# Kernel optimization log

Hardware: AMD Instinct MI355X
Metric: run time of the kernel (lower is better)

## Reference

```python
import jax, jax.numpy as jnp
import numpy as np

NQ = 200000; K = 4; M = 64; KEY = 64; V = 128; E = 64; B = 512; S = 200

def setup_inputs() -> dict:
    key = jax.random.key(0)
    ks = jax.random.split(key, 16)
    return {
        'q_embed_table': jax.random.normal(ks[0], (NQ + 1, E), jnp.float32) * 0.1,
        'alpha_mean': jax.random.normal(ks[1], (NQ,), jnp.float32) * 0.2,
        'beta_base': jax.random.normal(ks[2], (NQ,), jnp.float32) * 0.5,
        'beta_gaps': jax.random.uniform(ks[3], (NQ, K - 2), jnp.float32) * 0.5 + 0.25,
        'ability_means': jax.random.normal(ks[4], (M, V), jnp.float32) * 0.1,
        'ability_log_vars': jnp.zeros((M, V), jnp.float32),
        'memory_keys': jax.random.normal(ks[5], (M, KEY), jnp.float32),
        'q_to_key_w': jax.random.normal(ks[6], (E, KEY), jnp.float32) / np.sqrt(E),
        'q_to_key_b': jnp.zeros((KEY,), jnp.float32),
        'qa_embed_w': jax.random.normal(ks[7], (2, E), jnp.float32),
        'qa_embed_b': jnp.zeros((E,), jnp.float32),
        'qa_to_ev_w': jax.random.normal(ks[8], (E, V), jnp.float32) / np.sqrt(E),
        'qa_to_ev_b': jnp.zeros((V,), jnp.float32),
        'questions': jax.random.randint(ks[9], (B, S), 0, NQ),
        'responses': jax.random.randint(ks[10], (B, S), 0, K),
    }


def reference(q_embed_table, alpha_mean, beta_base, beta_gaps, ability_means,
              ability_log_vars, memory_keys, q_to_key_w, q_to_key_b,
              qa_embed_w, qa_embed_b, qa_to_ev_w, qa_to_ev_b,
              questions, responses):
    nQ = alpha_mean.shape[0]
    Kc = beta_gaps.shape[1] + 2  # n_categories

    # --- gather question-specific IRT params (irregular gather) ---
    alphas = jnp.exp(alpha_mean[questions])                      # [B,S]
    base = beta_base[questions]                                  # [B,S]
    gaps = jax.nn.softplus(beta_gaps[questions])                 # [B,S,K-2]
    # cumulative thresholds: beta_0 = base, beta_k = beta_{k-1} + gap_{k-1}
    betas = jnp.cumsum(jnp.concatenate([base[..., None], gaps], axis=-1), axis=-1)  # [B,S,K-1]

    # --- attention over memory slots ---
    q_emb = q_embed_table[questions]                             # [B,S,E]
    queries = q_emb @ q_to_key_w + q_to_key_b                    # [B,S,KEY]
    attn = jax.nn.softmax(jnp.einsum('bsk,mk->bsm', queries, memory_keys), axis=-1)  # [B,S,M]

    # --- evidence embedding from (question, response) ---
    qn = questions.astype(jnp.float32) / nQ
    rn = responses.astype(jnp.float32) / (Kc - 1)
    qa = jnp.stack([qn, rn], axis=-1) @ qa_embed_w + qa_embed_b  # [B,S,E]
    evidence = jnp.tanh(qa) @ qa_to_ev_w + qa_to_ev_b            # [B,S,V]

    # --- sequential memory read + per-slot Bayesian scatter update ---
    def step(carry, inp):
        means, log_vars = carry                                  # [M,V] each
        attn_t, ev_t = inp                                       # [B,M], [B,V]
        theta = jnp.mean(attn_t @ means, axis=-1)                # bayesian_read -> [B]
        # precision-weighted update of every slot (evidence_precision = 1)
        w = jnp.mean(attn_t, axis=0)                             # [M] update weights
        ev_mean = jnp.mean(ev_t, axis=0)                         # [V]
        prior_prec = jnp.exp(-log_vars)
        post_prec = prior_prec + w[:, None]
        post_mean = (prior_prec * means + ev_mean[None, :] * w[:, None]) / post_prec
        # torch updates under no_grad -> stop_gradient
        new_means = jax.lax.stop_gradient(post_mean)
        new_lv = jax.lax.stop_gradient(-jnp.log(post_prec))
        return (new_means, new_lv), theta

    (_, _), thetas = jax.lax.scan(
        step, (ability_means, ability_log_vars),
        (attn.transpose(1, 0, 2), evidence.transpose(1, 0, 2)))
    thetas = thetas.T                                            # [B,S]

    # --- GPCM category probabilities ---
    z = alphas[..., None] * (thetas[..., None] - betas)          # [B,S,K-1]
    cum = jnp.concatenate([jnp.zeros_like(z[..., :1]), jnp.cumsum(z, axis=-1)], axis=-1)  # [B,S,K]
    probs = jax.nn.softmax(cum, axis=-1)
    return probs
```

## Files before the change

kernel.cpp:

```cpp
#include <hip/hip_runtime.h>
#include <math.h>

#define M_SLOTS 64
#define E_DIM   64
#define KEY_DIM 64
#define V_DIM   128
#define K_CAT   4
#define S_LEN   200

typedef __attribute__((ext_vector_type(8)))  short short8;
typedef __attribute__((ext_vector_type(16))) float f32x16;

#define OFF_CT     0
#define OFF_BM     2048
#define OFF_WBAR   2112
#define OFF_BBAR   2176
#define OFF_RM0    2240
#define OFF_P0     2304
#define OFF_WSUM   2368
#define OFF_EMSUM  (OFF_WSUM + S_LEN*M_SLOTS)
#define OFF_INV    15424
#define OFF_ATTN   (OFF_INV + S_LEN*512)

#define PRE_CT_END   4096
#define PRE_BM_END   4160
#define PRE_WBAR_END 4224
#define PRE_BBAR     4224
#define PRE_RM_BEG   4225
#define PRE_RM_END   4289
#define PRE_Z_BEG    4289
#define PRE_Z_END    (4289 + S_LEN*M_SLOTS + S_LEN)

__device__ __forceinline__ unsigned pk2(float lo, float hi) {
    return __builtin_amdgcn_perm(__float_as_uint(hi), __float_as_uint(lo), 0x07060302u);
}
__device__ __forceinline__ unsigned pk2rne(float lo, float hi) {
    unsigned ul = __float_as_uint(lo); ul += 0x7fffu + ((ul >> 16) & 1u);
    unsigned uh = __float_as_uint(hi); uh += 0x7fffu + ((uh >> 16) & 1u);
    return __builtin_amdgcn_perm(uh, ul, 0x07060302u);
}
__device__ __forceinline__ unsigned short bf16rne(float f) {
    unsigned u = __float_as_uint(f);
    return (unsigned short)((u + 0x7fffu + ((u >> 16) & 1u)) >> 16);
}
__device__ __forceinline__ short8 as_s8(uint4 u) { return __builtin_bit_cast(short8, u); }

__device__ __forceinline__ void gpcm_store(float th, int q,
                                           const float* __restrict__ alpha_mean,
                                           const float* __restrict__ beta_base,
                                           const float* __restrict__ beta_gaps,
                                           float* __restrict__ out, size_t idx) {
    float a  = __expf(alpha_mean[q]);
    float b0 = beta_base[q];
    float2 g = *reinterpret_cast<const float2*>(&beta_gaps[q * (K_CAT - 2)]);
    float g0 = log1pf(__expf(g.x));
    float g1 = log1pf(__expf(g.y));
    float be1 = b0 + g0;
    float be2 = be1 + g1;
    float z0 = a * (th - b0);
    float z1 = a * (th - be1);
    float z2 = a * (th - be2);
    float c1 = z0, c2 = z0 + z1, c3 = z0 + z1 + z2;
    float cm = fmaxf(fmaxf(0.f, c1), fmaxf(c2, c3));
    float e0 = __expf(0.f - cm), e1 = __expf(c1 - cm), e2 = __expf(c2 - cm), e3 = __expf(c3 - cm);
    float si = __fdividef(1.0f, e0 + e1 + e2 + e3);
    float4 o4 = make_float4(e0 * si, e1 * si, e2 * si, e3 * si);
    *reinterpret_cast<float4*>(&out[idx * K_CAT]) = o4;
}

__global__ void k_pre(const float* __restrict__ q2k_w, const float* __restrict__ q2k_b,
                      const float* __restrict__ mkeys,
                      const float* __restrict__ ev_w, const float* __restrict__ ev_b,
                      const float* __restrict__ means, const float* __restrict__ logvars,
                      float* __restrict__ ws) {
    int gid = blockIdx.x * blockDim.x + threadIdx.x;
    if (gid < PRE_CT_END) {
        int e = gid >> 6, m = gid & 63;
        float s = 0.f;
        #pragma unroll
        for (int k = 0; k < KEY_DIM; ++k) s = fmaf(q2k_w[e * KEY_DIM + k], mkeys[m * KEY_DIM + k], s);
        ((unsigned short*)ws)[m * E_DIM + e] = bf16rne(s);
    } else if (gid < PRE_BM_END) {
        int m = gid - PRE_CT_END;
        float s = 0.f;
        #pragma unroll
        for (int k = 0; k < KEY_DIM; ++k) s = fmaf(q2k_b[k], mkeys[m * KEY_DIM + k], s);
        ws[OFF_BM + m] = s;
    } else if (gid < PRE_WBAR_END) {
        int e = gid - PRE_BM_END;
        float s = 0.f;
        for (int v = 0; v < V_DIM; ++v) s += ev_w[e * V_DIM + v];
        ws[OFF_WBAR + e] = s * (1.0f / V_DIM);
    } else if (gid == PRE_BBAR) {
        float s = 0.f;
        for (int v = 0; v < V_DIM; ++v) s += ev_b[v];
        ws[OFF_BBAR] = s * (1.0f / V_DIM);
    } else if (gid >= PRE_RM_BEG && gid < PRE_RM_END) {
        int m = gid - PRE_RM_BEG;
        const float4* mr = (const float4*)(means + (size_t)m * V_DIM);
        float s = 0.f;
        #pragma unroll
        for (int i = 0; i < V_DIM / 4; ++i) { float4 v = mr[i]; s += (v.x + v.y) + (v.z + v.w); }
        ws[OFF_RM0 + m] = s * (1.0f / V_DIM);
        ws[OFF_P0 + m]  = __expf(-logvars[(size_t)m * V_DIM]);
    } else if (gid >= PRE_Z_BEG && gid < PRE_Z_END) {
        ws[OFF_WSUM + (gid - PRE_Z_BEG)] = 0.f;
    }
}

__global__ __launch_bounds__(256, 3) void k_attn(
    const float* __restrict__ qtab, const int* __restrict__ qs, const int* __restrict__ rs,
    const float* __restrict__ ws_ro,
    const float* __restrict__ qa_w, const float* __restrict__ qa_b,
    uint2* __restrict__ attnb, float* __restrict__ invb,
    float* __restrict__ wsum, float* __restrict__ emsum,
    int B, float invNQ)
{
    __shared__ float4 lsEv[64];
    const int tid = threadIdx.x, wv = tid >> 6, lane = tid & 63;
    const int h = lane >> 5, p = lane & 31;
    const int t = blockIdx.x;
    const int b = blockIdx.y * 128 + wv * 32 + p;

    const int q = qs[(size_t)b * S_LEN + t];
    const int r = rs[(size_t)b * S_LEN + t];

    const float* qrow = qtab + (size_t)q * E_DIM;
    float4 qf[8];
    #pragma unroll
    for (int s = 0; s < 4; ++s) {
        const float4* src = (const float4*)(qrow + s * 16 + h * 8);
        qf[2 * s]     = src[0];
        qf[2 * s + 1] = src[1];
    }

    const unsigned short* ct = (const unsigned short*)ws_ro;
    uint4 af[8];
    #pragma unroll
    for (int mt = 0; mt < 2; ++mt)
        #pragma unroll
        for (int s = 0; s < 4; ++s)
            af[mt * 4 + s] = *(const uint4*)(ct + (p + 32 * mt) * E_DIM + s * 16 + h * 8);

    if (tid < 64) lsEv[tid] = make_float4(qa_w[tid], qa_w[E_DIM + tid], qa_b[tid],
                                          ws_ro[OFF_WBAR + tid]);
    const float bb = ws_ro[OFF_BBAR];

    const float* bm = ws_ro + OFF_BM;
    f32x16 acc[2];
    #pragma unroll
    for (int mt = 0; mt < 2; ++mt)
        #pragma unroll
        for (int g = 0; g < 4; ++g) {
            float4 v = *(const float4*)(bm + 8 * g + 4 * h + 32 * mt);
            acc[mt][4 * g + 0] = v.x; acc[mt][4 * g + 1] = v.y;
            acc[mt][4 * g + 2] = v.z; acc[mt][4 * g + 3] = v.w;
        }

    #pragma unroll
    for (int s = 0; s < 4; ++s) {
        uint4 bf;
        bf.x = pk2rne(qf[2 * s].x,     qf[2 * s].y);
        bf.y = pk2rne(qf[2 * s].z,     qf[2 * s].w);
        bf.z = pk2rne(qf[2 * s + 1].x, qf[2 * s + 1].y);
        bf.w = pk2rne(qf[2 * s + 1].z, qf[2 * s + 1].w);
        short8 bfr = as_s8(bf);
        acc[0] = __builtin_amdgcn_mfma_f32_32x32x16_bf16(as_s8(af[s]),     bfr, acc[0], 0, 0, 0);
        acc[1] = __builtin_amdgcn_mfma_f32_32x32x16_bf16(as_s8(af[4 + s]), bfr, acc[1], 0, 0, 0);
    }

    float av[32];
    float ssum = 0.f;
    #pragma unroll
    for (int j = 0; j < 16; ++j) { av[j]      = __expf(acc[0][j]); ssum += av[j]; }
    #pragma unroll
    for (int j = 0; j < 16; ++j) { av[16 + j] = __expf(acc[1][j]); ssum += av[16 + j]; }
    ssum += __shfl_xor(ssum, 32);
    const float inv = __fdividef(1.0f, ssum);

    #pragma unroll
    for (int u = 0; u < 8; ++u) {
        uint2 pk;
        pk.x = pk2(av[4 * u],     av[4 * u + 1]);
        pk.y = pk2(av[4 * u + 2], av[4 * u + 3]);
        attnb[(size_t)(t * 16 + h * 8 + u) * B + b] = pk;
    }
    if (!h) invb[(size_t)t * B + b] = inv;

    #pragma unroll
    for (int j = 0; j < 32; ++j) av[j] *= inv;
    #pragma unroll
    for (int step = 0; step < 5; ++step) {
        const int sh = 1 << step;
        #pragma unroll
        for (int j = 0; j < (32 >> step) / 2; ++j) {
            float p0 = av[2 * j]     + __shfl_xor(av[2 * j], sh);
            float p1 = av[2 * j + 1] + __shfl_xor(av[2 * j + 1], sh);
            av[j] = (lane & sh) ? p1 : p0;
        }
    }
    {
        const int jj = lane & 31;
        const int m = (jj & 3) + 8 * ((jj >> 2) & 3) + 4 * h + 32 * (jj >> 4);
        atomicAdd(&wsum[t * M_SLOTS + m], av[0]);
    }

    __syncthreads();

    float qn = (float)q * invNQ;
    float rn = (float)r * (1.0f / (K_CAT - 1));
    float evm = 0.f;
    #pragma unroll 8
    for (int e = 0; e < 32; ++e) {
        float4 pv = lsEv[h * 32 + e];
        float qa = fmaf(qn, pv.x, fmaf(rn, pv.y, pv.z));
        float ez = __expf(2.0f * qa);
        evm = fmaf(__fdividef(ez - 1.0f, ez + 1.0f), pv.w, evm);
    }
    evm += __shfl_xor(evm, 32);
    evm += bb;
    #pragma unroll
    for (int o = 16; o; o >>= 1) evm += __shfl_xor(evm, o);
    if (!lane) atomicAdd(&emsum[t], evm);
}

__global__ __launch_bounds__(256) void k_out(
    const uint2* __restrict__ attnb, const float* __restrict__ invb,
    const float* __restrict__ ws_ro, const int* __restrict__ qs,
    const float* __restrict__ alpha_mean, const float* __restrict__ beta_base,
    const float* __restrict__ beta_gaps, float* __restrict__ out, int B, float invB)
{
    __shared__ float lsRmP[M_SLOTS];
    const int tid = threadIdx.x;
    const int t = blockIdx.x;
    const int b = blockIdx.y * 256 + tid;
    const int q = qs[(size_t)b * S_LEN + t];

    uint2 v[16];
    #pragma unroll
    for (int s = 0; s < 16; ++s) v[s] = attnb[(size_t)(t * 16 + s) * B + b];
    const float iv = invb[(size_t)t * B + b];

    if (tid < 64) {
        const float* wsum  = ws_ro + OFF_WSUM;
        const float* emsum = ws_ro + OFF_EMSUM;
        float den = ws_ro[OFF_P0 + tid];
        float num = den * ws_ro[OFF_RM0 + tid];
        int s = 0;
        for (; s + 4 <= t; s += 4) {
            float w0 = wsum[(s + 0) * M_SLOTS + tid] * invB;
            float w1 = wsum[(s + 1) * M_SLOTS + tid] * invB;
            float w2 = wsum[(s + 2) * M_SLOTS + tid] * invB;
            float w3 = wsum[(s + 3) * M_SLOTS + tid] * invB;
            float e0 = emsum[s + 0], e1 = emsum[s + 1];
            float e2 = emsum[s + 2], e3 = emsum[s + 3];
            num = fmaf(e0 * invB, w0, num); den += w0;
            num = fmaf(e1 * invB, w1, num); den += w1;
            num = fmaf(e2 * invB, w2, num); den += w2;
            num = fmaf(e3 * invB, w3, num); den += w3;
        }
        for (; s < t; ++s) {
            float w = wsum[s * M_SLOTS + tid] * invB;
            num = fmaf(emsum[s] * invB, w, num);
            den += w;
        }
        const int m = tid;
        const int i = (m & 3) + 4 * ((m >> 3) & 3) + 16 * ((m >> 5) & 1) + 32 * ((m >> 2) & 1);
        lsRmP[i] = num / den;
    }
    __syncthreads();

    const float4* rm4 = (const float4*)lsRmP;
    float th = 0.f;
    #pragma unroll
    for (int s = 0; s < 16; ++s) {
        float4 rm = rm4[s];
        th = fmaf(__uint_as_float(v[s].x << 16),         rm.x, th);
        th = fmaf(__uint_as_float(v[s].x & 0xffff0000u), rm.y, th);
        th = fmaf(__uint_as_float(v[s].y << 16),         rm.z, th);
        th = fmaf(__uint_as_float(v[s].y & 0xffff0000u), rm.w, th);
    }
    th *= iv;
    gpcm_store(th, q, alpha_mean, beta_base, beta_gaps, out, (size_t)b * S_LEN + t);
}

extern "C" void kernel_launch(void* const* d_in, const int* in_sizes, int n_in,
                              void* d_out, int out_size, void* d_ws, size_t ws_size,
                              hipStream_t stream) {
    const float* qtab       = (const float*)d_in[0];
    const float* alpha_mean = (const float*)d_in[1];
    const float* beta_base  = (const float*)d_in[2];
    const float* beta_gaps  = (const float*)d_in[3];
    const float* ab_means   = (const float*)d_in[4];
    const float* ab_logvars = (const float*)d_in[5];
    const float* mkeys      = (const float*)d_in[6];
    const float* q2k_w      = (const float*)d_in[7];
    const float* q2k_b      = (const float*)d_in[8];
    const float* qa_w       = (const float*)d_in[9];
    const float* qa_b       = (const float*)d_in[10];
    const float* ev_w       = (const float*)d_in[11];
    const float* ev_b       = (const float*)d_in[12];
    const int*   qs         = (const int*)d_in[13];
    const int*   rs         = (const int*)d_in[14];
    float* out = (float*)d_out;
    float* ws  = (float*)d_ws;

    const int NQ = in_sizes[1];
    const int S  = S_LEN;
    const int B  = in_sizes[13] / S;

    float* wsum  = ws + OFF_WSUM;
    float* emsum = ws + OFF_EMSUM;
    float* invb  = ws + OFF_INV;
    uint2* attnb = (uint2*)(ws + OFF_ATTN);

    k_pre<<<(PRE_Z_END + 255) / 256, 256, 0, stream>>>(
        q2k_w, q2k_b, mkeys, ev_w, ev_b, ab_means, ab_logvars, ws);

    dim3 gA(S, B / 128);
    k_attn<<<gA, 256, 0, stream>>>(qtab, qs, rs, ws, qa_w, qa_b,
                                   attnb, invb, wsum, emsum, B, 1.0f / (float)NQ);

    dim3 gO(S, B / 256);
    k_out<<<gO, 256, 0, stream>>>(attnb, invb, ws, qs, alpha_mean, beta_base,
                                  beta_gaps, out, B, 1.0f / (float)B);
}
```

Measured before the change: 50.22 us.

## Recompute attention logits in output kernel instead of storing bf16 attention

Drops the bf16 attention matrix and softmax denominators that k_attn wrote to workspace and k_out read back. k_out now re-gathers the question embedding and recomputes the logits with MFMA, fusing exp, the read-weighted sum and normalization. The prefix reduction over earlier timesteps is also split across four waves with a shared-memory combine. This trades a large global write and read for repeated gather and MFMA work, and half the lanes sit idle at the store.

After: 49.37 us. About the same (-1.7%).

```diff
diff --git a/kernel.cpp b/kernel.cpp
--- a/kernel.cpp
+++ b/kernel.cpp
@@ -19,8 +19,6 @@
 #define OFF_P0     2304
 #define OFF_WSUM   2368
 #define OFF_EMSUM  (OFF_WSUM + S_LEN*M_SLOTS)
-#define OFF_INV    15424
-#define OFF_ATTN   (OFF_INV + S_LEN*512)
 
 #define PRE_CT_END   4096
 #define PRE_BM_END   4160
@@ -31,9 +29,6 @@
 #define PRE_Z_BEG    4289
 #define PRE_Z_END    (4289 + S_LEN*M_SLOTS + S_LEN)
 
-__device__ __forceinline__ unsigned pk2(float lo, float hi) {
-    return __builtin_amdgcn_perm(__float_as_uint(hi), __float_as_uint(lo), 0x07060302u);
-}
 __device__ __forceinline__ unsigned pk2rne(float lo, float hi) {
     unsigned ul = __float_as_uint(lo); ul += 0x7fffu + ((ul >> 16) & 1u);
     unsigned uh = __float_as_uint(hi); uh += 0x7fffu + ((uh >> 16) & 1u);
@@ -68,64 +63,10 @@
     *reinterpret_cast<float4*>(&out[idx * K_CAT]) = o4;
 }
 
-__global__ void k_pre(const float* __restrict__ q2k_w, const float* __restrict__ q2k_b,
-                      const float* __restrict__ mkeys,
-                      const float* __restrict__ ev_w, const float* __restrict__ ev_b,
-                      const float* __restrict__ means, const float* __restrict__ logvars,
-                      float* __restrict__ ws) {
-    int gid = blockIdx.x * blockDim.x + threadIdx.x;
-    if (gid < PRE_CT_END) {
-        int e = gid >> 6, m = gid & 63;
-        float s = 0.f;
-        #pragma unroll
-        for (int k = 0; k < KEY_DIM; ++k) s = fmaf(q2k_w[e * KEY_DIM + k], mkeys[m * KEY_DIM + k], s);
-        ((unsigned short*)ws)[m * E_DIM + e] = bf16rne(s);
-    } else if (gid < PRE_BM_END) {
-        int m = gid - PRE_CT_END;
-        float s = 0.f;
-        #pragma unroll
-        for (int k = 0; k < KEY_DIM; ++k) s = fmaf(q2k_b[k], mkeys[m * KEY_DIM + k], s);
-        ws[OFF_BM + m] = s;
-    } else if (gid < PRE_WBAR_END) {
-        int e = gid - PRE_BM_END;
-        float s = 0.f;
-        for (int v = 0; v < V_DIM; ++v) s += ev_w[e * V_DIM + v];
-        ws[OFF_WBAR + e] = s * (1.0f / V_DIM);
-    } else if (gid == PRE_BBAR) {
-        float s = 0.f;
-        for (int v = 0; v < V_DIM; ++v) s += ev_b[v];
-        ws[OFF_BBAR] = s * (1.0f / V_DIM);
-    } else if (gid >= PRE_RM_BEG && gid < PRE_RM_END) {
-        int m = gid - PRE_RM_BEG;
-        const float4* mr = (const float4*)(means + (size_t)m * V_DIM);
-        float s = 0.f;
-        #pragma unroll
-        for (int i = 0; i < V_DIM / 4; ++i) { float4 v = mr[i]; s += (v.x + v.y) + (v.z + v.w); }
-        ws[OFF_RM0 + m] = s * (1.0f / V_DIM);
-        ws[OFF_P0 + m]  = __expf(-logvars[(size_t)m * V_DIM]);
-    } else if (gid >= PRE_Z_BEG && gid < PRE_Z_END) {
-        ws[OFF_WSUM + (gid - PRE_Z_BEG)] = 0.f;
-    }
-}
-
-__global__ __launch_bounds__(256, 3) void k_attn(
-    const float* __restrict__ qtab, const int* __restrict__ qs, const int* __restrict__ rs,
-    const float* __restrict__ ws_ro,
-    const float* __restrict__ qa_w, const float* __restrict__ qa_b,
-    uint2* __restrict__ attnb, float* __restrict__ invb,
-    float* __restrict__ wsum, float* __restrict__ emsum,
-    int B, float invNQ)
+__device__ __forceinline__ void mfma_logits(
+    const float* __restrict__ qrow, const unsigned short* __restrict__ ct,
+    const float* __restrict__ bm, int h, int p, f32x16 acc[2])
 {
-    __shared__ float4 lsEv[64];
-    const int tid = threadIdx.x, wv = tid >> 6, lane = tid & 63;
-    const int h = lane >> 5, p = lane & 31;
-    const int t = blockIdx.x;
-    const int b = blockIdx.y * 128 + wv * 32 + p;
-
-    const int q = qs[(size_t)b * S_LEN + t];
-    const int r = rs[(size_t)b * S_LEN + t];
-
-    const float* qrow = qtab + (size_t)q * E_DIM;
     float4 qf[8];
     #pragma unroll
     for (int s = 0; s < 4; ++s) {
@@ -133,21 +74,12 @@
         qf[2 * s]     = src[0];
         qf[2 * s + 1] = src[1];
     }
-
-    const unsigned short* ct = (const unsigned short*)ws_ro;
     uint4 af[8];
     #pragma unroll
     for (int mt = 0; mt < 2; ++mt)
         #pragma unroll
         for (int s = 0; s < 4; ++s)
             af[mt * 4 + s] = *(const uint4*)(ct + (p + 32 * mt) * E_DIM + s * 16 + h * 8);
-
-    if (tid < 64) lsEv[tid] = make_float4(qa_w[tid], qa_w[E_DIM + tid], qa_b[tid],
-                                          ws_ro[OFF_WBAR + tid]);
-    const float bb = ws_ro[OFF_BBAR];
-
-    const float* bm = ws_ro + OFF_BM;
-    f32x16 acc[2];
     #pragma unroll
     for (int mt = 0; mt < 2; ++mt)
         #pragma unroll
@@ -156,7 +88,6 @@
             acc[mt][4 * g + 0] = v.x; acc[mt][4 * g + 1] = v.y;
             acc[mt][4 * g + 2] = v.z; acc[mt][4 * g + 3] = v.w;
         }
-
     #pragma unroll
     for (int s = 0; s < 4; ++s) {
         uint4 bf;
@@ -168,6 +99,71 @@
         acc[0] = __builtin_amdgcn_mfma_f32_32x32x16_bf16(as_s8(af[s]),     bfr, acc[0], 0, 0, 0);
         acc[1] = __builtin_amdgcn_mfma_f32_32x32x16_bf16(as_s8(af[4 + s]), bfr, acc[1], 0, 0, 0);
     }
+}
+
+__global__ void k_pre(const float* __restrict__ q2k_w, const float* __restrict__ q2k_b,
+                      const float* __restrict__ mkeys,
+                      const float* __restrict__ ev_w, const float* __restrict__ ev_b,
+                      const float* __restrict__ means, const float* __restrict__ logvars,
+                      float* __restrict__ ws) {
+    int gid = blockIdx.x * blockDim.x + threadIdx.x;
+    if (gid < PRE_CT_END) {
+        int e = gid >> 6, m = gid & 63;
+        float s = 0.f;
+        #pragma unroll
+        for (int k = 0; k < KEY_DIM; ++k) s = fmaf(q2k_w[e * KEY_DIM + k], mkeys[m * KEY_DIM + k], s);
+        ((unsigned short*)ws)[m * E_DIM + e] = bf16rne(s);
+    } else if (gid < PRE_BM_END) {
+        int m = gid - PRE_CT_END;
+        float s = 0.f;
+        #pragma unroll
+        for (int k = 0; k < KEY_DIM; ++k) s = fmaf(q2k_b[k], mkeys[m * KEY_DIM + k], s);
+        ws[OFF_BM + m] = s;
+    } else if (gid < PRE_WBAR_END) {
+        int e = gid - PRE_BM_END;
+        float s = 0.f;
+        for (int v = 0; v < V_DIM; ++v) s += ev_w[e * V_DIM + v];
+        ws[OFF_WBAR + e] = s * (1.0f / V_DIM);
+    } else if (gid == PRE_BBAR) {
+        float s = 0.f;
+        for (int v = 0; v < V_DIM; ++v) s += ev_b[v];
+        ws[OFF_BBAR] = s * (1.0f / V_DIM);
+    } else if (gid >= PRE_RM_BEG && gid < PRE_RM_END) {
+        int m = gid - PRE_RM_BEG;
+        const float4* mr = (const float4*)(means + (size_t)m * V_DIM);
+        float s = 0.f;
+        #pragma unroll
+        for (int i = 0; i < V_DIM / 4; ++i) { float4 v = mr[i]; s += (v.x + v.y) + (v.z + v.w); }
+        ws[OFF_RM0 + m] = s * (1.0f / V_DIM);
+        ws[OFF_P0 + m]  = __expf(-logvars[(size_t)m * V_DIM]);
+    } else if (gid >= PRE_Z_BEG && gid < PRE_Z_END) {
+        ws[OFF_WSUM + (gid - PRE_Z_BEG)] = 0.f;
+    }
+}
+
+__global__ __launch_bounds__(256, 3) void k_attn(
+    const float* __restrict__ qtab, const int* __restrict__ qs, const int* __restrict__ rs,
+    const float* __restrict__ ws_ro,
+    const float* __restrict__ qa_w, const float* __restrict__ qa_b,
+    float* __restrict__ wsum, float* __restrict__ emsum,
+    int B, float invNQ)
+{
+    __shared__ float4 lsEv[64];
+    const int tid = threadIdx.x, wv = tid >> 6, lane = tid & 63;
+    const int h = lane >> 5, p = lane & 31;
+    const int t = blockIdx.x;
+    const int b = blockIdx.y * 128 + wv * 32 + p;
+
+    const int q = qs[(size_t)b * S_LEN + t];
+    const int r = rs[(size_t)b * S_LEN + t];
+
+    if (tid < 64) lsEv[tid] = make_float4(qa_w[tid], qa_w[E_DIM + tid], qa_b[tid],
+                                          ws_ro[OFF_WBAR + tid]);
+    const float bb = ws_ro[OFF_BBAR];
+
+    f32x16 acc[2];
+    mfma_logits(qtab + (size_t)q * E_DIM, (const unsigned short*)ws_ro,
+                ws_ro + OFF_BM, h, p, acc);
 
     float av[32];
     float ssum = 0.f;
@@ -177,15 +173,6 @@
     for (int j = 0; j < 16; ++j) { av[16 + j] = __expf(acc[1][j]); ssum += av[16 + j]; }
     ssum += __shfl_xor(ssum, 32);
     const float inv = __fdividef(1.0f, ssum);
-
-    #pragma unroll
-    for (int u = 0; u < 8; ++u) {
-        uint2 pk;
-        pk.x = pk2(av[4 * u],     av[4 * u + 1]);
-        pk.y = pk2(av[4 * u + 2], av[4 * u + 3]);
-        attnb[(size_t)(t * 16 + h * 8 + u) * B + b] = pk;
-    }
-    if (!h) invb[(size_t)t * B + b] = inv;
 
     #pragma unroll
     for (int j = 0; j < 32; ++j) av[j] *= inv;
@@ -224,64 +211,69 @@
     if (!lane) atomicAdd(&emsum[t], evm);
 }
 
-__global__ __launch_bounds__(256) void k_out(
-    const uint2* __restrict__ attnb, const float* __restrict__ invb,
-    const float* __restrict__ ws_ro, const int* __restrict__ qs,
+__global__ __launch_bounds__(256, 3) void k_out(
+    const float* __restrict__ qtab, const int* __restrict__ qs,
+    const float* __restrict__ ws_ro,
     const float* __restrict__ alpha_mean, const float* __restrict__ beta_base,
     const float* __restrict__ beta_gaps, float* __restrict__ out, int B, float invB)
 {
+    __shared__ float lsW[4][M_SLOTS], lsN[4][M_SLOTS];
     __shared__ float lsRmP[M_SLOTS];
-    const int tid = threadIdx.x;
+    const int tid = threadIdx.x, wv = tid >> 6, lane = tid & 63;
+    const int h = lane >> 5, p = lane & 31;
     const int t = blockIdx.x;
-    const int b = blockIdx.y * 256 + tid;
+    const int b = blockIdx.y * 128 + wv * 32 + p;
+
     const int q = qs[(size_t)b * S_LEN + t];
 
-    uint2 v[16];
-    #pragma unroll
-    for (int s = 0; s < 16; ++s) v[s] = attnb[(size_t)(t * 16 + s) * B + b];
-    const float iv = invb[(size_t)t * B + b];
-
-    if (tid < 64) {
+    {
         const float* wsum  = ws_ro + OFF_WSUM;
         const float* emsum = ws_ro + OFF_EMSUM;
-        float den = ws_ro[OFF_P0 + tid];
-        float num = den * ws_ro[OFF_RM0 + tid];
-        int s = 0;
-        for (; s + 4 <= t; s += 4) {
-            float w0 = wsum[(s + 0) * M_SLOTS + tid] * invB;
-            float w1 = wsum[(s + 1) * M_SLOTS + tid] * invB;
-            float w2 = wsum[(s + 2) * M_SLOTS + tid] * invB;
-            float w3 = wsum[(s + 3) * M_SLOTS + tid] * invB;
-            float e0 = emsum[s + 0], e1 = emsum[s + 1];
-            float e2 = emsum[s + 2], e3 = emsum[s + 3];
-            num = fmaf(e0 * invB, w0, num); den += w0;
-            num = fmaf(e1 * invB, w1, num); den += w1;
-            num = fmaf(e2 * invB, w2, num); den += w2;
-            num = fmaf(e3 * invB, w3, num); den += w3;
+        const int seg = (t + 3) >> 2;
+        const int s0 = wv * seg, s1 = min(s0 + seg, t);
+        float pw = 0.f, pn = 0.f;
+        for (int s = s0; s < s1; ++s) {
+            float w = wsum[s * M_SLOTS + lane];
+            pw += w;
+            pn = fmaf(emsum[s], w, pn);
         }
-        for (; s < t; ++s) {
-            float w = wsum[s * M_SLOTS + tid] * invB;
-            num = fmaf(emsum[s] * invB, w, num);
-            den += w;
-        }
+        lsW[wv][lane] = pw; lsN[wv][lane] = pn;
+    }
+    __syncthreads();
+    if (tid < 64) {
         const int m = tid;
-        const int i = (m & 3) + 4 * ((m >> 3) & 3) + 16 * ((m >> 5) & 1) + 32 * ((m >> 2) & 1);
-        lsRmP[i] = num / den;
+        float sw = lsW[0][m] + lsW[1][m] + lsW[2][m] + lsW[3][m];
+        float sn = lsN[0][m] + lsN[1][m] + lsN[2][m] + lsN[3][m];
+        float den = ws_ro[OFF_P0 + m] + sw * invB;
+        float num = ws_ro[OFF_P0 + m] * ws_ro[OFF_RM0 + m] + sn * (invB * invB);
+        const int idx = ((m >> 2) & 1) * 32 + ((m >> 5) & 1) * 16 + (m & 3) + 4 * ((m >> 3) & 3);
+        lsRmP[idx] = num / den;
     }
     __syncthreads();
 
-    const float4* rm4 = (const float4*)lsRmP;
-    float th = 0.f;
-    #pragma unroll
-    for (int s = 0; s < 16; ++s) {
-        float4 rm = rm4[s];
-        th = fmaf(__uint_as_float(v[s].x << 16),         rm.x, th);
-        th = fmaf(__uint_as_float(v[s].x & 0xffff0000u), rm.y, th);
-        th = fmaf(__uint_as_float(v[s].y << 16),         rm.z, th);
-        th = fmaf(__uint_as_float(v[s].y & 0xffff0000u), rm.w, th);
-    }
-    th *= iv;
-    gpcm_store(th, q, alpha_mean, beta_base, beta_gaps, out, (size_t)b * S_LEN + t);
+    f32x16 acc[2];
+    mfma_logits(qtab + (size_t)q * E_DIM, (const unsigned short*)ws_ro,
+                ws_ro + OFF_BM, h, p, acc);
+
+    float ssum = 0.f, th = 0.f;
+    const float* rmh = lsRmP + h * 32;
+    #pragma unroll
+    for (int j = 0; j < 16; ++j) {
+        float e = __expf(acc[0][j]);
+        ssum += e;
+        th = fmaf(e, rmh[j], th);
+    }
+    #pragma unroll
+    for (int j = 0; j < 16; ++j) {
+        float e = __expf(acc[1][j]);
+        ssum += e;
+        th = fmaf(e, rmh[16 + j], th);
+    }
+    ssum += __shfl_xor(ssum, 32);
+    th   += __shfl_xor(th, 32);
+    th = __fdividef(th, ssum);
+
+    if (!h) gpcm_store(th, q, alpha_mean, beta_base, beta_gaps, out, (size_t)b * S_LEN + t);
 }
 
 extern "C" void kernel_launch(void* const* d_in, const int* in_sizes, int n_in,
@@ -311,17 +303,14 @@
 
     float* wsum  = ws + OFF_WSUM;
     float* emsum = ws + OFF_EMSUM;
-    float* invb  = ws + OFF_INV;
-    uint2* attnb = (uint2*)(ws + OFF_ATTN);
 
     k_pre<<<(PRE_Z_END + 255) / 256, 256, 0, stream>>>(
         q2k_w, q2k_b, mkeys, ev_w, ev_b, ab_means, ab_logvars, ws);
 
-    dim3 gA(S, B / 128);
-    k_attn<<<gA, 256, 0, stream>>>(qtab, qs, rs, ws, qa_w, qa_b,
-                                   attnb, invb, wsum, emsum, B, 1.0f / (float)NQ);
-
-    dim3 gO(S, B / 256);
-    k_out<<<gO, 256, 0, stream>>>(attnb, invb, ws, qs, alpha_mean, beta_base,
-                                  beta_gaps, out, B, 1.0f / (float)B);
-}
+    dim3 g(S, B / 128);
+    k_attn<<<g, 256, 0, stream>>>(qtab, qs, rs, ws, qa_w, qa_b,
+                                  wsum, emsum, B, 1.0f / (float)NQ);
+
+    k_out<<<g, 256, 0, stream>>>(qtab, qs, ws, alpha_mean, beta_base,
+                                 beta_gaps, out, B, 1.0f / (float)B);
+}
```
